# Optimization experiments

Measured on AMD Instinct MI355X. Metric: run time of the kernel, lower is better.

The kernel has to match this reference:

```python
import jax, jax.numpy as jnp
import numpy as np


def setup_inputs() -> dict:
    key = jax.random.key(0)
    ks = jax.random.split(key, 5)
    B, N, F, S = 8, 128, 32, 8
    F_ = 32          # output channels
    H = 32           # kernel_network hidden width
    node_features = jax.random.normal(ks[0], (B, N, F), dtype=jnp.float32)
    fltr = jax.random.uniform(ks[1], (B, N, N), dtype=jnp.float32)
    edge_features = jax.random.normal(ks[2], (B, N, N, S), dtype=jnp.float32)
    W0 = jax.random.normal(ks[3], (S, H), dtype=jnp.float32) * (1.0 / np.sqrt(S))
    b0 = jnp.zeros((H,), dtype=jnp.float32)
    W_out = jax.random.normal(ks[4], (H, F_ * F), dtype=jnp.float32) * (1.0 / np.sqrt(H))
    b_out = jnp.zeros((F_ * F,), dtype=jnp.float32)
    bias = jnp.zeros((F_,), dtype=jnp.float32)
    return {"node_features": node_features, "fltr": fltr, "edge_features": edge_features,
            "W0": W0, "b0": b0, "W_out": W_out, "b_out": b_out, "bias": bias}


def reference(node_features, fltr, edge_features, W0, b0, W_out, b_out, bias):
    B, N, F = node_features.shape
    F_ = bias.shape[0]
    # row-normalize the filter (adjacency)
    fltr_n = fltr / jnp.maximum(jnp.sum(fltr, axis=-1, keepdims=True), 1e-11)
    # kernel-generating network over edge features: (B,N,N,S) -> (B,N,N,F_*F)
    h = jax.nn.relu(edge_features @ W0 + b0)
    kernel = (h @ W_out + b_out).reshape(B, N, N, F_, F)
    # scale by normalized filter and aggregate neighbors:
    # out[a,b,c] = sum_{i,f} fltr_n[a,b,i] * kernel[a,b,i,c,f] * nf[a,i,f]
    out = jnp.einsum('abi,abicf,aif->abc', fltr_n, kernel, node_features)
    out = out + bias  # (B,N,F_)
    return out
```

## Files before the change

### kernel.cpp

```cpp
#include <hip/hip_runtime.h>

#define Bn 8
#define Nn 128
#define Fdim 32
#define Sdim 8
#define Hdim 32
#define Fout 32

__global__ __launch_bounds__(256, 4) void ecc_kernel(
    const float* __restrict__ nf,
    const float* __restrict__ fltr,
    const float* __restrict__ ef,
    const float* __restrict__ W0,
    const float* __restrict__ b0,
    const float* __restrict__ Wout,
    const float* __restrict__ bout,
    const float* __restrict__ bias,
    float* __restrict__ out)
{
    __shared__ __align__(16) float nf_s[Nn * Fdim];
    __shared__ __align__(16) float hbuf[Nn * Hdim];
    __shared__ __align__(16) float efs[Nn * Sdim];
    __shared__ __align__(16) float qp[Nn];
    __shared__ float fn_s[Nn];
    __shared__ float inv_s;

    const int t    = threadIdx.x;
    const int blk  = blockIdx.x;
    const int a    = blk >> 7;
    const int hcol = t & 31;

    float w0r[8];
    #pragma unroll
    for (int s = 0; s < Sdim; ++s) w0r[s] = W0[s * Hdim + hcol];
    const float b0r = b0[hcol];

    {
        const float4* nsrc = (const float4*)(nf + (size_t)a * Nn * Fdim);
        float4* ndst = (float4*)nf_s;
        #pragma unroll
        for (int j = 0; j < 4; ++j) ndst[j * 256 + t] = nsrc[j * 256 + t];
        ((float4*)efs)[t] = ((const float4*)(ef + (size_t)blk * Nn * Sdim))[t];
    }
    if (t < Nn) fn_s[t] = fltr[(size_t)blk * Nn + t];
    __syncthreads();

    if (t < 64) {
        float s = fn_s[t] + fn_s[t + 64];
        #pragma unroll
        for (int off = 32; off > 0; off >>= 1) s += __shfl_down(s, off);
        if (t == 0) inv_s = 1.0f / fmaxf(s, 1e-11f);
    }

    {
        const int il = t >> 5;
        #pragma unroll 4
        for (int k = 0; k < 16; ++k) {
            const int i = il * 16 + k;
            const float4 e0 = *(const float4*)&efs[i * Sdim];
            const float4 e1 = *(const float4*)&efs[i * Sdim + 4];
            float acc = b0r;
            acc += e0.x * w0r[0] + e0.y * w0r[1] + e0.z * w0r[2] + e0.w * w0r[3];
            acc += e1.x * w0r[4] + e1.y * w0r[5] + e1.z * w0r[6] + e1.w * w0r[7];
            hbuf[i * Hdim + hcol] = fmaxf(acc, 0.0f) * fn_s[i];
        }
    }
    __syncthreads();

    const int fq   = t & 7;
    const int h0   = ((t >> 3) & 15) * 2;
    const int half = t >> 7;
    float4 acc0 = make_float4(0.f, 0.f, 0.f, 0.f);
    float4 acc1 = make_float4(0.f, 0.f, 0.f, 0.f);
    {
        const int ibase = half * 64;
        #pragma unroll 8
        for (int k = 0; k < 64; ++k) {
            const int i = ibase + k;
            const float2 hv = *(const float2*)&hbuf[i * Hdim + h0];
            const float4 nv = *(const float4*)&nf_s[i * Fdim + fq * 4];
            acc0.x += hv.x * nv.x; acc0.y += hv.x * nv.y;
            acc0.z += hv.x * nv.z; acc0.w += hv.x * nv.w;
            acc1.x += hv.y * nv.x; acc1.y += hv.y * nv.y;
            acc1.z += hv.y * nv.z; acc1.w += hv.y * nv.w;
        }
    }
    if (half) {
        float4* p = (float4*)&efs[(t - 128) * 8];
        p[0] = acc0; p[1] = acc1;
    }
    __syncthreads();

    if (!half) {
        const float4* p = (const float4*)&efs[t * 8];
        const float4 p0 = p[0], p1 = p[1];
        acc0.x += p0.x; acc0.y += p0.y; acc0.z += p0.z; acc0.w += p0.w;
        acc1.x += p1.x; acc1.y += p1.y; acc1.z += p1.z; acc1.w += p1.w;
        *(float4*)&hbuf[h0 * Fdim + fq * 4]       = acc0;
        *(float4*)&hbuf[(h0 + 1) * Fdim + fq * 4] = acc1;
    } else {
        const int f = t & 31, qr = (t >> 5) & 3;
        float q = 0.f;
        #pragma unroll 4
        for (int k = 0; k < 32; ++k) {
            const int i = qr * 32 + k;
            q += fn_s[i] * nf_s[i * Fdim + f];
        }
        qp[qr * 32 + f] = q;
    }
    __syncthreads();

    {
        const int c = t >> 3, f4 = t & 7;
        const float* wbase = Wout + (size_t)c * Fdim + f4 * 4;
        float partial = 0.f;
        #pragma unroll 8
        for (int h = 0; h < Hdim; ++h) {
            const float4 wv = *(const float4*)(wbase + (size_t)h * (Fout * Fdim));
            const float4 tv = *(const float4*)&hbuf[h * Fdim + f4 * 4];
            partial += tv.x * wv.x + tv.y * wv.y + tv.z * wv.z + tv.w * wv.w;
        }
        {
            const float4 q0 = *(const float4*)&qp[f4 * 4];
            const float4 q1 = *(const float4*)&qp[32 + f4 * 4];
            const float4 q2 = *(const float4*)&qp[64 + f4 * 4];
            const float4 q3 = *(const float4*)&qp[96 + f4 * 4];
            const float4 bv = *(const float4*)(bout + (size_t)c * Fdim + f4 * 4);
            partial += (q0.x + q1.x + q2.x + q3.x) * bv.x;
            partial += (q0.y + q1.y + q2.y + q3.y) * bv.y;
            partial += (q0.z + q1.z + q2.z + q3.z) * bv.z;
            partial += (q0.w + q1.w + q2.w + q3.w) * bv.w;
        }
        partial += __shfl_down(partial, 4, 8);
        partial += __shfl_down(partial, 2, 8);
        partial += __shfl_down(partial, 1, 8);
        if (f4 == 0)
            out[(size_t)blk * Fout + c] = partial * inv_s + bias[c];
    }
}

extern "C" void kernel_launch(void* const* d_in, const int* in_sizes, int n_in,
                              void* d_out, int out_size, void* d_ws, size_t ws_size,
                              hipStream_t stream) {
    const float* nf   = (const float*)d_in[0];
    const float* fltr = (const float*)d_in[1];
    const float* ef   = (const float*)d_in[2];
    const float* W0   = (const float*)d_in[3];
    const float* b0   = (const float*)d_in[4];
    const float* Wout = (const float*)d_in[5];
    const float* bout = (const float*)d_in[6];
    const float* bias = (const float*)d_in[7];
    float* out = (float*)d_out;

    ecc_kernel<<<dim3(Bn * Nn), dim3(256), 0, stream>>>(
        nf, fltr, ef, W0, b0, Wout, bout, bias, out);
}
```

Before: 80.74 us.

## Compute h^T·nf contraction with bf16 MFMA and transposed padded LDS tiles

Replaces the scalar FP32 outer-product loop that formed T[h,f] = sum_i h[i,h]*nf[i,f] with a bf16 MFMA 16x16x32 contraction. Operands are converted to bf16 and stored transposed in padded LDS buffers. Inputs are read straight from global memory rather than staged through shared memory first. This removes several syncs and the split-half reduction, shrinks LDS use, and trades some precision by rounding to bf16.

```diff
diff --git a/kernel.cpp b/kernel.cpp
--- a/kernel.cpp
+++ b/kernel.cpp
@@ -6,6 +6,19 @@
 #define Sdim 8
 #define Hdim 32
 #define Fout 32
+
+typedef float  f32x4  __attribute__((ext_vector_type(4)));
+typedef short  bf16x8 __attribute__((ext_vector_type(8)));
+
+#define PITCH 136
+
+__device__ __forceinline__ unsigned short f2bf(float x) {
+    union { float f; unsigned u; } v; v.f = x;
+    return (unsigned short)((v.u + 0x7FFFu + ((v.u >> 16) & 1u)) >> 16);
+}
+__device__ __forceinline__ unsigned pack2(float lo, float hi) {
+    return (unsigned)f2bf(lo) | ((unsigned)f2bf(hi) << 16);
+}
 
 __global__ __launch_bounds__(256, 4) void ecc_kernel(
     const float* __restrict__ nf,
@@ -18,11 +31,10 @@
     const float* __restrict__ bias,
     float* __restrict__ out)
 {
-    __shared__ __align__(16) float nf_s[Nn * Fdim];
-    __shared__ __align__(16) float hbuf[Nn * Hdim];
-    __shared__ __align__(16) float efs[Nn * Sdim];
+    __shared__ __align__(16) unsigned short hT[Hdim * PITCH];
+    __shared__ __align__(16) unsigned short nT[Fdim * PITCH];
+    __shared__ __align__(16) float Ts[Hdim * 36];
     __shared__ __align__(16) float qp[Nn];
-    __shared__ float fn_s[Nn];
     __shared__ float inv_s;
 
     const int t    = threadIdx.x;
@@ -30,83 +42,81 @@
     const int a    = blk >> 7;
     const int hcol = t & 31;
 
-    float w0r[8];
+    const float* __restrict__ nfa  = nf   + (size_t)a   * (Nn * Fdim);
+    const float* __restrict__ frow = fltr + (size_t)blk * Nn;
+    const float* __restrict__ erow = ef   + (size_t)blk * (Nn * Sdim);
+
+    float w0r[Sdim];
     #pragma unroll
     for (int s = 0; s < Sdim; ++s) w0r[s] = W0[s * Hdim + hcol];
     const float b0r = b0[hcol];
 
-    {
-        const float4* nsrc = (const float4*)(nf + (size_t)a * Nn * Fdim);
-        float4* ndst = (float4*)nf_s;
-        #pragma unroll
-        for (int j = 0; j < 4; ++j) ndst[j * 256 + t] = nsrc[j * 256 + t];
-        ((float4*)efs)[t] = ((const float4*)(ef + (size_t)blk * Nn * Sdim))[t];
-    }
-    if (t < Nn) fn_s[t] = fltr[(size_t)blk * Nn + t];
-    __syncthreads();
-
     if (t < 64) {
-        float s = fn_s[t] + fn_s[t + 64];
+        float s = frow[t] + frow[t + 64];
         #pragma unroll
         for (int off = 32; off > 0; off >>= 1) s += __shfl_down(s, off);
         if (t == 0) inv_s = 1.0f / fmaxf(s, 1e-11f);
     }
 
     {
-        const int il = t >> 5;
+        const int f = t & 31, iseg = t >> 5;
+        unsigned* dst = (unsigned*)&nT[f * PITCH + iseg * 16];
         #pragma unroll 4
-        for (int k = 0; k < 16; ++k) {
-            const int i = il * 16 + k;
-            const float4 e0 = *(const float4*)&efs[i * Sdim];
-            const float4 e1 = *(const float4*)&efs[i * Sdim + 4];
-            float acc = b0r;
-            acc += e0.x * w0r[0] + e0.y * w0r[1] + e0.z * w0r[2] + e0.w * w0r[3];
-            acc += e1.x * w0r[4] + e1.y * w0r[5] + e1.z * w0r[6] + e1.w * w0r[7];
-            hbuf[i * Hdim + hcol] = fmaxf(acc, 0.0f) * fn_s[i];
+        for (int k = 0; k < 16; k += 2) {
+            const int i = iseg * 16 + k;
+            const float x0 = nfa[i * Fdim + f];
+            const float x1 = nfa[(i + 1) * Fdim + f];
+            dst[k >> 1] = pack2(x0, x1);
         }
     }
-    __syncthreads();
 
-    const int fq   = t & 7;
-    const int h0   = ((t >> 3) & 15) * 2;
-    const int half = t >> 7;
-    float4 acc0 = make_float4(0.f, 0.f, 0.f, 0.f);
-    float4 acc1 = make_float4(0.f, 0.f, 0.f, 0.f);
     {
-        const int ibase = half * 64;
-        #pragma unroll 8
-        for (int k = 0; k < 64; ++k) {
-            const int i = ibase + k;
-            const float2 hv = *(const float2*)&hbuf[i * Hdim + h0];
-            const float4 nv = *(const float4*)&nf_s[i * Fdim + fq * 4];
-            acc0.x += hv.x * nv.x; acc0.y += hv.x * nv.y;
-            acc0.z += hv.x * nv.z; acc0.w += hv.x * nv.w;
-            acc1.x += hv.y * nv.x; acc1.y += hv.y * nv.y;
-            acc1.z += hv.y * nv.z; acc1.w += hv.y * nv.w;
+        const int il = t >> 5;
+        unsigned* dst = (unsigned*)&hT[hcol * PITCH + il * 16];
+        #pragma unroll 2
+        for (int k = 0; k < 16; k += 2) {
+            const int i0 = il * 16 + k;
+            const float4 e0a = *(const float4*)(erow + i0 * Sdim);
+            const float4 e0b = *(const float4*)(erow + i0 * Sdim + 4);
+            const float4 e1a = *(const float4*)(erow + i0 * Sdim + 8);
+            const float4 e1b = *(const float4*)(erow + i0 * Sdim + 12);
+            float a0 = b0r, a1 = b0r;
+            a0 += e0a.x * w0r[0] + e0a.y * w0r[1] + e0a.z * w0r[2] + e0a.w * w0r[3];
+            a0 += e0b.x * w0r[4] + e0b.y * w0r[5] + e0b.z * w0r[6] + e0b.w * w0r[7];
+            a1 += e1a.x * w0r[0] + e1a.y * w0r[1] + e1a.z * w0r[2] + e1a.w * w0r[3];
+            a1 += e1b.x * w0r[4] + e1b.y * w0r[5] + e1b.z * w0r[6] + e1b.w * w0r[7];
+            const float h0 = fmaxf(a0, 0.0f) * frow[i0];
+            const float h1 = fmaxf(a1, 0.0f) * frow[i0 + 1];
+            dst[k >> 1] = pack2(h0, h1);
         }
     }
-    if (half) {
-        float4* p = (float4*)&efs[(t - 128) * 8];
-        p[0] = acc0; p[1] = acc1;
-    }
-    __syncthreads();
 
-    if (!half) {
-        const float4* p = (const float4*)&efs[t * 8];
-        const float4 p0 = p[0], p1 = p[1];
-        acc0.x += p0.x; acc0.y += p0.y; acc0.z += p0.z; acc0.w += p0.w;
-        acc1.x += p1.x; acc1.y += p1.y; acc1.z += p1.z; acc1.w += p1.w;
-        *(float4*)&hbuf[h0 * Fdim + fq * 4]       = acc0;
-        *(float4*)&hbuf[(h0 + 1) * Fdim + fq * 4] = acc1;
-    } else {
+    if (t >= 128) {
         const int f = t & 31, qr = (t >> 5) & 3;
         float q = 0.f;
         #pragma unroll 4
         for (int k = 0; k < 32; ++k) {
             const int i = qr * 32 + k;
-            q += fn_s[i] * nf_s[i * Fdim + f];
+            q += frow[i] * nfa[i * Fdim + f];
         }
         qp[qr * 32 + f] = q;
+    }
+    __syncthreads();
+
+    {
+        const int w  = t >> 6, l = t & 63;
+        const int lr = l & 15, lg = l >> 4;
+        const int mt = w >> 1, nt = w & 1;
+        f32x4 acc = {0.f, 0.f, 0.f, 0.f};
+        #pragma unroll
+        for (int kt = 0; kt < 4; ++kt) {
+            const bf16x8 av = *(const bf16x8*)&hT[(mt * 16 + lr) * PITCH + kt * 32 + lg * 8];
+            const bf16x8 bv = *(const bf16x8*)&nT[(nt * 16 + lr) * PITCH + kt * 32 + lg * 8];
+            acc = __builtin_amdgcn_mfma_f32_16x16x32_bf16(av, bv, acc, 0, 0, 0);
+        }
+        #pragma unroll
+        for (int r = 0; r < 4; ++r)
+            Ts[(mt * 16 + lg * 4 + r) * 36 + nt * 16 + lr] = acc[r];
     }
     __syncthreads();
 
@@ -117,7 +127,7 @@
         #pragma unroll 8
         for (int h = 0; h < Hdim; ++h) {
             const float4 wv = *(const float4*)(wbase + (size_t)h * (Fout * Fdim));
-            const float4 tv = *(const float4*)&hbuf[h * Fdim + f4 * 4];
+            const float4 tv = *(const float4*)&Ts[h * 36 + f4 * 4];
             partial += tv.x * wv.x + tv.y * wv.y + tv.z * wv.z + tv.w * wv.w;
         }
         {
```

Measured after the change: 80.89 us. About the same (+0.2%).
